# Performance work log

Hardware: AMD Instinct MI355X
Metric: run time of the kernel (lower is better)

## Reference

```python
import jax, jax.numpy as jnp
import numpy as np

B, C, H, W = 2, 256, 48, 48
NH = 8
HD = C // NH  # 32
T = H * W    # 2304


def setup_inputs() -> dict:
    keys = jax.random.split(jax.random.key(0), 16)
    s = lambda fan: 1.0 / np.sqrt(fan)
    x = jax.random.normal(keys[0], (B, C, H, W), jnp.float32)
    wq = jax.random.normal(keys[1], (C, C), jnp.float32) * s(C)
    bq = jax.random.normal(keys[2], (C,), jnp.float32) * 0.01
    wk = jax.random.normal(keys[3], (C, C), jnp.float32) * s(C)
    bk = jax.random.normal(keys[4], (C,), jnp.float32) * 0.01
    wv = jax.random.normal(keys[5], (C, C), jnp.float32) * s(C)
    bv = jax.random.normal(keys[6], (C,), jnp.float32) * 0.01
    wo = jax.random.normal(keys[7], (C, C), jnp.float32) * s(C)
    bo = jax.random.normal(keys[8], (C,), jnp.float32) * 0.01
    gamma1 = jnp.ones((C,), jnp.float32)
    beta1 = jnp.zeros((C,), jnp.float32)
    w1 = jax.random.normal(keys[9], (4 * C, C), jnp.float32) * s(C)
    bf1 = jax.random.normal(keys[10], (4 * C,), jnp.float32) * 0.01
    w2 = jax.random.normal(keys[11], (C, 4 * C), jnp.float32) * s(4 * C)
    bf2 = jax.random.normal(keys[12], (C,), jnp.float32) * 0.01
    gamma2 = jnp.ones((C,), jnp.float32)
    beta2 = jnp.zeros((C,), jnp.float32)
    return dict(x=x, wq=wq, bq=bq, wk=wk, bk=bk, wv=wv, bv=bv, wo=wo, bo=bo,
                gamma1=gamma1, beta1=beta1, w1=w1, bf1=bf1, w2=w2, bf2=bf2,
                gamma2=gamma2, beta2=beta2)


def group_norm1(x, gamma, beta, eps=1e-5):
    # GroupNorm(1, C): normalize over (C, H, W) per sample, per-channel affine.
    mu = jnp.mean(x, axis=(1, 2, 3), keepdims=True)
    var = jnp.mean((x - mu) ** 2, axis=(1, 2, 3), keepdims=True)
    xn = (x - mu) * jax.lax.rsqrt(var + eps)
    return xn * gamma[None, :, None, None] + beta[None, :, None, None]


def reference(x, wq, bq, wk, bk, wv, bv, wo, bo, gamma1, beta1,
              w1, bf1, w2, bf2, gamma2, beta2):
    b, c, h, w = x.shape
    t = h * w
    xt = x.reshape(b, c, t).transpose(0, 2, 1)  # [b, t, c]
    # 1x1 conv == per-token linear
    def heads(y):
        return y.reshape(b, t, NH, HD).transpose(0, 2, 1, 3)  # [b, nh, t, hd]
    q = heads(xt @ wq.T + bq)
    k = heads(xt @ wk.T + bk)
    v = heads(xt @ wv.T + bv)
    # flash SDPA runs in fp16 with fp32 accumulation
    q16 = q.astype(jnp.float16)
    k16 = k.astype(jnp.float16)
    v16 = v.astype(jnp.float16)
    scale = 1.0 / np.sqrt(HD)
    scores = jnp.einsum('bhqd,bhkd->bhqk', q16.astype(jnp.float32),
                        k16.astype(jnp.float32)) * scale
    attn = jax.nn.softmax(scores, axis=-1)
    out = jnp.einsum('bhqk,bhkd->bhqd', attn,
                     v16.astype(jnp.float32)).astype(jnp.float16)
    # remove component along normalized v (fp16, like torch code)
    vn = v16 / jnp.maximum(
        jnp.sqrt(jnp.sum(v16 * v16, axis=-1, keepdims=True)),
        jnp.float16(1e-12))
    out = out - jnp.sum(out * vn, axis=-1, keepdims=True) * vn
    out = out.astype(x.dtype)
    out = out.transpose(0, 2, 1, 3).reshape(b, t, c)  # [b, t, c]
    out = out @ wo.T + bo
    out = out.transpose(0, 2, 1).reshape(b, c, h, w)
    x1 = group_norm1(x + out, gamma1, beta1)
    # FFN: 1x1 conv -> relu -> 1x1 conv, per token
    x1t = x1.reshape(b, c, t).transpose(0, 2, 1)  # [b, t, c]
    hdn = jax.nn.relu(x1t @ w1.T + bf1)
    ffn = (hdn @ w2.T + bf2).transpose(0, 2, 1).reshape(b, c, h, w)
    x2 = group_norm1(x1 + ffn, gamma2, beta2)
    return x2
```

## Files before the change

### kernel.cpp

```cpp
#include <hip/hip_runtime.h>
#include <hip/hip_fp16.h>

typedef _Float16 f16x8 __attribute__((ext_vector_type(8)));
typedef __fp16 fp16x2 __attribute__((ext_vector_type(2)));
typedef float f32x4 __attribute__((ext_vector_type(4)));

namespace {

constexpr int B = 2, C = 256, T = 2304, F = 1024, NH = 8, HD = 32;
constexpr int BH = B * NH;
constexpr int NCHUNK = 4;
constexpr int CHUNK = T / NCHUNK;
constexpr float C2 = 0.17677669529663687f * 1.4426950408889634f;
constexpr float INV_N = 1.0f / (float)(C * T);

constexpr size_t N_WQKV = (size_t)3 * C * C;
constexpr size_t N_WO   = (size_t)C * C;
constexpr size_t N_W1   = (size_t)F * C;
constexpr size_t N_W2   = (size_t)C * F;
constexpr size_t N_WALL = N_WQKV + N_WO + N_W1 + N_W2;

constexpr size_t OFF_QKV  = 0;
constexpr size_t SZ_QKV   = (size_t)B * 3 * C * T * 2;
constexpr size_t OFF_AO   = OFF_QKV + SZ_QKV;
constexpr size_t SZ_AO    = (size_t)B * C * T * 2;
constexpr size_t OFF_X1   = OFF_AO + SZ_AO;
constexpr size_t SZ_X1    = (size_t)B * C * T * 4;
constexpr size_t OFF_PART = OFF_X1 + SZ_X1;
constexpr size_t SZ_OP    = (size_t)NCHUNK * BH * HD * T * 2;
constexpr size_t SZ_MP    = (size_t)NCHUNK * BH * T * 4;
constexpr size_t OFF_OP   = OFF_PART;
constexpr size_t OFF_MP   = OFF_OP + SZ_OP;
constexpr size_t OFF_LP   = OFF_MP + SZ_MP;
constexpr size_t SZ_H16   = (size_t)B * F * T * 2;
constexpr size_t SZ_PART  = SZ_OP + 2 * SZ_MP;
constexpr size_t SZ_UNION = SZ_PART > SZ_H16 ? SZ_PART : SZ_H16;
constexpr size_t OFF_H16  = OFF_PART;
constexpr size_t OFF_W16  = OFF_PART + SZ_UNION;
constexpr size_t OFF_BQKV = OFF_W16 + N_WALL * 2;
constexpr size_t OFF_STATS = OFF_BQKV + (size_t)3 * C * 4;

}

__global__ __launch_bounds__(256)
void convert_weights(const float* __restrict__ wq, const float* __restrict__ wk,
                     const float* __restrict__ wv, const float* __restrict__ wo,
                     const float* __restrict__ w1, const float* __restrict__ w2,
                     const float* __restrict__ bq, const float* __restrict__ bk,
                     const float* __restrict__ bv,
                     _Float16* __restrict__ w16, float* __restrict__ bqkv,
                     float* __restrict__ stats)
{
  const size_t tid = (size_t)blockIdx.x * 256 + threadIdx.x;
  if (tid < 8) stats[tid] = 0.f;
  if (tid < 3 * C)
    bqkv[tid] = tid < C ? bq[tid] : (tid < 2 * C ? bk[tid - C] : bv[tid - 2 * C]);
  for (size_t i4 = tid; i4 < N_WALL / 4; i4 += (size_t)gridDim.x * 256) {
    const size_t e = i4 * 4;
    const float* src;
    if      (e < 65536)  src = wq + e;
    else if (e < 131072) src = wk + (e - 65536);
    else if (e < 196608) src = wv + (e - 131072);
    else if (e < 262144) src = wo + (e - 196608);
    else if (e < 524288) src = w1 + (e - 262144);
    else                 src = w2 + (e - 524288);
    const float4 v = *(const float4*)src;
    union { _Float16 h[4]; uint2 u; } pk;
    pk.h[0] = (_Float16)v.x; pk.h[1] = (_Float16)v.y;
    pk.h[2] = (_Float16)v.z; pk.h[3] = (_Float16)v.w;
    *(uint2*)(w16 + e) = pk.u;
  }
}

template<bool RELU, bool RES, bool GNIN, bool GNRES, bool STATS,
         typename InT, typename OutT>
__global__ __launch_bounds__(256)
void gemm_mfma(const _Float16* __restrict__ W, const InT* __restrict__ X,
               const float* __restrict__ bias, const float* __restrict__ res,
               OutT* __restrict__ out, int CO, int K,
               const float* __restrict__ stats_in,
               const float* __restrict__ gamma, const float* __restrict__ beta,
               float* __restrict__ stats_out)
{
  const int b   = blockIdx.z;
  const int co0 = blockIdx.y * 64;
  const int t0  = blockIdx.x * 64;
  const int tid = threadIdx.x;
  const int wid = tid >> 6, lane = tid & 63;
  const int g = lane >> 4, lo = lane & 15;
  const int wm = wid & 1, wn = wid >> 1;

  __shared__ f16x8 xs[2][4][64];
  __shared__ float gs[256], bs[256];
  __shared__ float red[8];

  float mu = 0.f, rsig = 0.f;
  if (GNIN || GNRES) {
    const float s1 = stats_in[b * 2], s2 = stats_in[b * 2 + 1];
    mu = s1 * INV_N;
    rsig = rsqrtf(s2 * INV_N - mu * mu + 1e-5f);
  }
  if (GNIN) { gs[tid] = gamma[tid]; bs[tid] = beta[tid]; }

  const f32x4 z4 = {0.f, 0.f, 0.f, 0.f};
  f32x4 acc00 = z4, acc01 = z4, acc10 = z4, acc11 = z4;

  const int st = tid & 63;
  const int kp = tid >> 6;
  const InT* Xp = X + (size_t)b * K * T + t0 + st;
  const _Float16* Wp = W + (size_t)(co0 + wm * 32 + lo) * K + 8 * g;

  float xr[8];
#pragma unroll
  for (int j = 0; j < 8; ++j) xr[j] = (float)Xp[(size_t)(kp * 8 + j) * T];
  f16x8 afc0 = *(const f16x8*)(Wp);
  f16x8 afc1 = *(const f16x8*)(Wp + (size_t)16 * K);

  __syncthreads();

  int it = 0;
  for (int k0 = 0; k0 < K; k0 += 32, ++it) {
    const int buf = it & 1;
    union { fp16x2 h2[4]; f16x8 v8; } u;
#pragma unroll
    for (int j2 = 0; j2 < 4; ++j2) {
      float v0 = xr[2 * j2], v1 = xr[2 * j2 + 1];
      if (GNIN) {
        const int k = k0 + kp * 8 + 2 * j2;
        v0 = (v0 - mu) * rsig * gs[k] + bs[k];
        v1 = (v1 - mu) * rsig * gs[k + 1] + bs[k + 1];
      }
      u.h2[j2] = __builtin_amdgcn_cvt_pkrtz(v0, v1);
    }
    xs[buf][kp][st] = u.v8;

    const int k1 = (k0 + 32 < K) ? k0 + 32 : k0;
#pragma unroll
    for (int j = 0; j < 8; ++j) xr[j] = (float)Xp[(size_t)(k1 + kp * 8 + j) * T];
    const f16x8 afn0 = *(const f16x8*)(Wp + (size_t)k1);
    const f16x8 afn1 = *(const f16x8*)(Wp + (size_t)16 * K + k1);

    __syncthreads();

    const f16x8 bf0 = xs[buf][g][wn * 32 + lo];
    const f16x8 bf1 = xs[buf][g][wn * 32 + 16 + lo];
    acc00 = __builtin_amdgcn_mfma_f32_16x16x32_f16(afc0, bf0, acc00, 0, 0, 0);
    acc01 = __builtin_amdgcn_mfma_f32_16x16x32_f16(afc0, bf1, acc01, 0, 0, 0);
    acc10 = __builtin_amdgcn_mfma_f32_16x16x32_f16(afc1, bf0, acc10, 0, 0, 0);
    acc11 = __builtin_amdgcn_mfma_f32_16x16x32_f16(afc1, bf1, acc11, 0, 0, 0);

    afc0 = afn0;
    afc1 = afn1;
  }

  float s = 0.f, ss = 0.f;
  const size_t obase = ((size_t)b * CO + co0 + wm * 32) * T + t0 + wn * 32 + lo;
  const float* resb = res + obase;
  OutT* outb = out + obase;
  const f32x4 accs[2][2] = {{acc00, acc01}, {acc10, acc11}};
#pragma unroll
  for (int mi = 0; mi < 2; ++mi) {
#pragma unroll
    for (int r = 0; r < 4; ++r) {
      const int row = mi * 16 + 4 * g + r;
      const int co = co0 + wm * 32 + row;
      const float bi = bias[co];
      float gm = 0.f, bt = 0.f;
      if (GNRES) { gm = gamma[co]; bt = beta[co]; }
#pragma unroll
      for (int ni = 0; ni < 2; ++ni) {
        float v = accs[mi][ni][r] + bi;
        if (RES) {
          float rv = resb[(size_t)row * T + ni * 16];
          if (GNRES) rv = (rv - mu) * rsig * gm + bt;
          v += rv;
        }
        if (RELU) v = fmaxf(v, 0.f);
        outb[(size_t)row * T + ni * 16] = (OutT)v;
        if (STATS) { s += v; ss = fmaf(v, v, ss); }
      }
    }
  }

  if (STATS) {
#pragma unroll
    for (int off = 32; off > 0; off >>= 1) {
      s  += __shfl_down(s, off);
      ss += __shfl_down(ss, off);
    }
    if (lane == 0) { red[wid] = s; red[4 + wid] = ss; }
    __syncthreads();
    if (tid == 0) {
      atomicAdd(&stats_out[b * 2],     red[0] + red[1] + red[2] + red[3]);
      atomicAdd(&stats_out[b * 2 + 1], red[4] + red[5] + red[6] + red[7]);
    }
  }
}

__global__ __launch_bounds__(512)
void attn_mfma(const _Float16* __restrict__ qkv, _Float16* __restrict__ opart,
               float* __restrict__ mpart, float* __restrict__ lpart)
{
  const int tid  = threadIdx.x;
  const int wid  = tid >> 6;
  const int lane = tid & 63;
  const int g    = lane >> 4;
  const int lo   = lane & 15;
  const int chunk = blockIdx.y;
  const int bh   = blockIdx.z;
  const int b    = bh >> 3, h = bh & 7;
  const int tq   = blockIdx.x * 128 + wid * 16 + lo;
  const size_t qb = ((size_t)b * 3 * C + h * HD) * T;
  const size_t kb = qb + (size_t)C * T;
  const size_t vb = qb + (size_t)2 * C * T;

  __shared__ _Float16 kt[2][64][36];
  __shared__ _Float16 vt[2][32][72];
  __shared__ _Float16 pl[8][16][72];

  const int t   = tid & 63;
  const int dp  = tid >> 6;
  const int dv  = tid >> 4;
  const int seg = tid & 15;

  f16x8 qf;
#pragma unroll
  for (int j = 0; j < 8; ++j)
    qf[j] = (_Float16)((float)qkv[qb + (size_t)(8 * g + j) * T + tq] * C2);

  const f32x4 zero4 = {0.f, 0.f, 0.f, 0.f};
  f32x4 oa[2] = {zero4, zero4};
  float m = -1e30f, l = 0.f;

  constexpr int NIT = CHUNK / 64;

  ushort ka[4];
  uint2  va;
  {
    const int tk0 = chunk * CHUNK;
#pragma unroll
    for (int dd = 0; dd < 4; ++dd)
      ka[dd] = *(const ushort*)(qkv + kb + (size_t)(dp * 4 + dd) * T + tk0 + t);
    va = *(const uint2*)(qkv + vb + (size_t)dv * T + tk0 + seg * 4);
  }

  for (int it = 0; it < NIT; ++it) {
    const int buf = it & 1;

    *(uint*)&kt[buf][t][dp * 4]     = (uint)ka[0] | ((uint)ka[1] << 16);
    *(uint*)&kt[buf][t][dp * 4 + 2] = (uint)ka[2] | ((uint)ka[3] << 16);
    *(uint2*)&vt[buf][dv][seg * 4] = va;

    {
      const int tkn = chunk * CHUNK + (it + 1 < NIT ? it + 1 : it) * 64;
      ushort ka2[4];
      uint2  va2;
#pragma unroll
      for (int dd = 0; dd < 4; ++dd)
        ka2[dd] = *(const ushort*)(qkv + kb + (size_t)(dp * 4 + dd) * T + tkn + t);
      va2 = *(const uint2*)(qkv + vb + (size_t)dv * T + tkn + seg * 4);

      __syncthreads();

      f32x4 s4[4];
#pragma unroll
      for (int mt = 0; mt < 4; ++mt) {
        union { f16x8 v; uint2 u[2]; } kf;
        const _Float16* kr = &kt[buf][mt * 16 + lo][8 * g];
        kf.u[0] = *(const uint2*)(kr);
        kf.u[1] = *(const uint2*)(kr + 4);
        s4[mt] = __builtin_amdgcn_mfma_f32_16x16x32_f16(kf.v, qf, zero4, 0, 0, 0);
      }
      float rmax = -1e30f;
#pragma unroll
      for (int mt = 0; mt < 4; ++mt) {
        const float m01 = fmaxf(s4[mt][0], s4[mt][1]);
        const float m23 = fmaxf(s4[mt][2], s4[mt][3]);
        rmax = fmaxf(rmax, fmaxf(m01, m23));
      }
      rmax = fmaxf(rmax, __shfl_xor(rmax, 16));
      rmax = fmaxf(rmax, __shfl_xor(rmax, 32));
      if (!__all(rmax <= m)) {
        const float mn = fmaxf(m, rmax);
        const float fsc = __builtin_amdgcn_exp2f(m - mn);
        m = mn;
        l *= fsc;
#pragma unroll
        for (int dt = 0; dt < 2; ++dt)
#pragma unroll
          for (int r = 0; r < 4; ++r) oa[dt][r] *= fsc;
      }
      float p[4][4];
      float psum = 0.f;
#pragma unroll
      for (int mt = 0; mt < 4; ++mt)
#pragma unroll
        for (int r = 0; r < 4; ++r) {
          p[mt][r] = __builtin_amdgcn_exp2f(s4[mt][r] - m);
          psum += p[mt][r];
        }
      psum += __shfl_xor(psum, 16);
      psum += __shfl_xor(psum, 32);
      l += psum;

#pragma unroll
      for (int mt = 0; mt < 4; ++mt) {
        union { fp16x2 h2[2]; uint2 u2; } pw;
        pw.h2[0] = __builtin_amdgcn_cvt_pkrtz(p[mt][0], p[mt][1]);
        pw.h2[1] = __builtin_amdgcn_cvt_pkrtz(p[mt][2], p[mt][3]);
        *(uint2*)&pl[wid][lo][16 * mt + 4 * g] = pw.u2;
      }
#pragma unroll
      for (int c2 = 0; c2 < 2; ++c2) {
        const f16x8 pbv = *(const f16x8*)&pl[wid][lo][c2 * 32 + 8 * g];
#pragma unroll
        for (int dt = 0; dt < 2; ++dt) {
          const f16x8 vf = *(const f16x8*)&vt[buf][dt * 16 + lo][c2 * 32 + 8 * g];
          oa[dt] = __builtin_amdgcn_mfma_f32_16x16x32_f16(vf, pbv, oa[dt], 0, 0, 0);
        }
      }

#pragma unroll
      for (int dd = 0; dd < 4; ++dd) ka[dd] = ka2[dd];
      va = va2;
    }
  }

  const float invL = 1.f / l;
  const size_t ob = (size_t)(chunk * BH + bh) * HD * T;
#pragma unroll
  for (int dt = 0; dt < 2; ++dt)
#pragma unroll
    for (int r = 0; r < 4; ++r)
      opart[ob + (size_t)(dt * 16 + 4 * g + r) * T + tq] =
          (_Float16)(oa[dt][r] * invL);
  if (g == 0) {
    const size_t pb = (size_t)(chunk * BH + bh) * T + tq;
    mpart[pb] = m;
    lpart[pb] = l;
  }
}

__global__ __launch_bounds__(64)
void attn_combine(const _Float16* __restrict__ opart, const float* __restrict__ mpart,
                  const float* __restrict__ lpart, const _Float16* __restrict__ qkv,
                  _Float16* __restrict__ AOh)
{
  const int q  = blockIdx.x * 64 + threadIdx.x;
  const int bh = blockIdx.y;
  const int b  = bh >> 3, h = bh & 7;
  float mv[NCHUNK], lv[NCHUNK];
  float M = -1e30f;
#pragma unroll
  for (int c = 0; c < NCHUNK; ++c) {
    const size_t pb = (size_t)(c * BH + bh) * T + q;
    mv[c] = mpart[pb];
    lv[c] = lpart[pb];
    M = fmaxf(M, mv[c]);
  }
  float L = 0.f;
  float wc[NCHUNK];
#pragma unroll
  for (int c = 0; c < NCHUNK; ++c) {
    wc[c] = __builtin_amdgcn_exp2f(mv[c] - M) * lv[c];
    L += wc[c];
  }
  const float inv = 1.f / L;
#pragma unroll
  for (int c = 0; c < NCHUNK; ++c) wc[c] *= inv;

  float o[HD];
#pragma unroll
  for (int d = 0; d < HD; ++d) o[d] = 0.f;
#pragma unroll
  for (int c = 0; c < NCHUNK; ++c) {
    const size_t ob = (size_t)(c * BH + bh) * HD * T + q;
#pragma unroll
    for (int d = 0; d < HD; ++d)
      o[d] = fmaf(wc[c], (float)opart[ob + (size_t)d * T], o[d]);
  }

  const size_t vbase = ((size_t)b * 3 * C + 2 * C + h * HD) * T + q;
  float vv[HD], nrm2 = 0.f;
#pragma unroll
  for (int d = 0; d < HD; ++d) {
    vv[d] = (float)qkv[vbase + (size_t)d * T];
    nrm2 = fmaf(vv[d], vv[d], nrm2);
  }
  const float nrm = fmaxf(sqrtf(nrm2), 1e-12f);
  float dot = 0.f;
  float o16[HD], vn[HD];
#pragma unroll
  for (int d = 0; d < HD; ++d) {
    o16[d] = (float)(_Float16)(o[d]);
    vn[d]  = (float)(_Float16)(vv[d] / nrm);
    dot = fmaf(o16[d], vn[d], dot);
  }
  const size_t ab = ((size_t)b * C + h * HD) * T + q;
#pragma unroll
  for (int d = 0; d < HD; ++d)
    AOh[ab + (size_t)d * T] = (_Float16)(o16[d] - dot * vn[d]);
}

__global__ __launch_bounds__(256)
void gn_norm(const float* __restrict__ Y, const float* __restrict__ stats,
             const float* __restrict__ gamma, const float* __restrict__ beta,
             float* __restrict__ O)
{
  const int i = blockIdx.x * 256 + threadIdx.x;
  const int b = i / (C * T);
  const int c = (i / T) & (C - 1);
  const float mu  = stats[b * 2] * INV_N;
  const float var = stats[b * 2 + 1] * INV_N - mu * mu;
  const float r = rsqrtf(var + 1e-5f);
  O[i] = (Y[i] - mu) * r * gamma[c] + beta[c];
}

extern "C" void kernel_launch(void* const* d_in, const int* in_sizes, int n_in,
                              void* d_out, int out_size, void* d_ws, size_t ws_size,
                              hipStream_t stream)
{
  const float* x      = (const float*)d_in[0];
  const float* wq     = (const float*)d_in[1];
  const float* bq     = (const float*)d_in[2];
  const float* wk     = (const float*)d_in[3];
  const float* bk     = (const float*)d_in[4];
  const float* wv     = (const float*)d_in[5];
  const float* bv     = (const float*)d_in[6];
  const float* wo     = (const float*)d_in[7];
  const float* bo     = (const float*)d_in[8];
  const float* gamma1 = (const float*)d_in[9];
  const float* beta1  = (const float*)d_in[10];
  const float* w1     = (const float*)d_in[11];
  const float* bf1    = (const float*)d_in[12];
  const float* w2     = (const float*)d_in[13];
  const float* bf2    = (const float*)d_in[14];
  const float* gamma2 = (const float*)d_in[15];
  const float* beta2  = (const float*)d_in[16];

  char* ws = (char*)d_ws;
  _Float16* qkv16 = (_Float16*)(ws + OFF_QKV);
  _Float16* ao16  = (_Float16*)(ws + OFF_AO);
  float*    x1    = (float*)(ws + OFF_X1);
  _Float16* opart = (_Float16*)(ws + OFF_OP);
  float*    mpart = (float*)(ws + OFF_MP);
  float*    lpart = (float*)(ws + OFF_LP);
  _Float16* h16   = (_Float16*)(ws + OFF_H16);
  _Float16* w16   = (_Float16*)(ws + OFF_W16);
  float*    bqkv  = (float*)(ws + OFF_BQKV);
  float*    stats = (float*)(ws + OFF_STATS);
  float*    out   = (float*)d_out;

  const _Float16* wqkv16 = w16;
  const _Float16* wo16   = w16 + N_WQKV;
  const _Float16* w116   = w16 + N_WQKV + N_WO;
  const _Float16* w216   = w16 + N_WQKV + N_WO + N_W1;

  const dim3 blk256(256);

  convert_weights<<<768, blk256, 0, stream>>>(wq, wk, wv, wo, w1, w2, bq, bk, bv,
                                              w16, bqkv, stats);

  gemm_mfma<false, false, false, false, false, float, _Float16>
      <<<dim3(36, 12, 2), blk256, 0, stream>>>(
          wqkv16, x, bqkv, nullptr, qkv16, 3 * C, C, nullptr, nullptr, nullptr, nullptr);

  attn_mfma<<<dim3(T / 128, NCHUNK, BH), dim3(512), 0, stream>>>(qkv16, opart, mpart, lpart);
  attn_combine<<<dim3(T / 64, BH), dim3(64), 0, stream>>>(opart, mpart, lpart, qkv16, ao16);

  gemm_mfma<false, true, false, false, true, _Float16, float>
      <<<dim3(36, 4, 2), blk256, 0, stream>>>(
          wo16, ao16, bo, x, x1, C, C, nullptr, nullptr, nullptr, stats);

  gemm_mfma<true, false, true, false, false, float, _Float16>
      <<<dim3(36, 16, 2), blk256, 0, stream>>>(
          w116, x1, bf1, nullptr, h16, F, C, stats, gamma1, beta1, nullptr);

  gemm_mfma<false, true, false, true, true, _Float16, float>
      <<<dim3(36, 4, 2), blk256, 0, stream>>>(
          w216, h16, bf2, x1, out, C, F, stats, gamma1, beta1, stats + 4);

  gn_norm<<<dim3(4608), blk256, 0, stream>>>(out, stats + 4, gamma2, beta2, out);
}
```

Before: 125.3 us.

## Drop weight-conversion kernel, convert fp32 weights in GEMM; retile small GEMMs

Removes the separate convert_weights launch. Each GEMM now reads fp32 weights directly and packs them to fp16 in registers before the MFMA, and the QKV GEMM picks wq/wk/wv per block so no concatenated buffer is needed. Stats zeroing moves into attn_combine. The two CO=256 GEMMs switch to 32-token tiles for twice as many blocks, and attention split-K goes from 4 to 6 chunks. The cost is that every GEMM block reads twice the weight bytes and does redundant conversions.

```diff
diff --git a/kernel.cpp b/kernel.cpp
--- a/kernel.cpp
+++ b/kernel.cpp
@@ -9,16 +9,10 @@
 
 constexpr int B = 2, C = 256, T = 2304, F = 1024, NH = 8, HD = 32;
 constexpr int BH = B * NH;
-constexpr int NCHUNK = 4;
+constexpr int NCHUNK = 6;
 constexpr int CHUNK = T / NCHUNK;
 constexpr float C2 = 0.17677669529663687f * 1.4426950408889634f;
 constexpr float INV_N = 1.0f / (float)(C * T);
-
-constexpr size_t N_WQKV = (size_t)3 * C * C;
-constexpr size_t N_WO   = (size_t)C * C;
-constexpr size_t N_W1   = (size_t)F * C;
-constexpr size_t N_W2   = (size_t)C * F;
-constexpr size_t N_WALL = N_WQKV + N_WO + N_W1 + N_W2;
 
 constexpr size_t OFF_QKV  = 0;
 constexpr size_t SZ_QKV   = (size_t)B * 3 * C * T * 2;
@@ -36,61 +30,43 @@
 constexpr size_t SZ_PART  = SZ_OP + 2 * SZ_MP;
 constexpr size_t SZ_UNION = SZ_PART > SZ_H16 ? SZ_PART : SZ_H16;
 constexpr size_t OFF_H16  = OFF_PART;
-constexpr size_t OFF_W16  = OFF_PART + SZ_UNION;
-constexpr size_t OFF_BQKV = OFF_W16 + N_WALL * 2;
-constexpr size_t OFF_STATS = OFF_BQKV + (size_t)3 * C * 4;
-
-}
-
+constexpr size_t OFF_STATS = OFF_PART + SZ_UNION;
+
+__device__ inline f16x8 cvt8(const float4 a, const float4 b)
+{
+  union { fp16x2 h2[4]; f16x8 v; } u;
+  u.h2[0] = __builtin_amdgcn_cvt_pkrtz(a.x, a.y);
+  u.h2[1] = __builtin_amdgcn_cvt_pkrtz(a.z, a.w);
+  u.h2[2] = __builtin_amdgcn_cvt_pkrtz(b.x, b.y);
+  u.h2[3] = __builtin_amdgcn_cvt_pkrtz(b.z, b.w);
+  return u.v;
+}
+
+}
+
+template<int TT, bool QKV3, bool RELU, bool RES, bool GNIN, bool GNRES,
+         bool STATS, typename InT, typename OutT>
 __global__ __launch_bounds__(256)
-void convert_weights(const float* __restrict__ wq, const float* __restrict__ wk,
-                     const float* __restrict__ wv, const float* __restrict__ wo,
-                     const float* __restrict__ w1, const float* __restrict__ w2,
-                     const float* __restrict__ bq, const float* __restrict__ bk,
-                     const float* __restrict__ bv,
-                     _Float16* __restrict__ w16, float* __restrict__ bqkv,
-                     float* __restrict__ stats)
-{
-  const size_t tid = (size_t)blockIdx.x * 256 + threadIdx.x;
-  if (tid < 8) stats[tid] = 0.f;
-  if (tid < 3 * C)
-    bqkv[tid] = tid < C ? bq[tid] : (tid < 2 * C ? bk[tid - C] : bv[tid - 2 * C]);
-  for (size_t i4 = tid; i4 < N_WALL / 4; i4 += (size_t)gridDim.x * 256) {
-    const size_t e = i4 * 4;
-    const float* src;
-    if      (e < 65536)  src = wq + e;
-    else if (e < 131072) src = wk + (e - 65536);
-    else if (e < 196608) src = wv + (e - 131072);
-    else if (e < 262144) src = wo + (e - 196608);
-    else if (e < 524288) src = w1 + (e - 262144);
-    else                 src = w2 + (e - 524288);
-    const float4 v = *(const float4*)src;
-    union { _Float16 h[4]; uint2 u; } pk;
-    pk.h[0] = (_Float16)v.x; pk.h[1] = (_Float16)v.y;
-    pk.h[2] = (_Float16)v.z; pk.h[3] = (_Float16)v.w;
-    *(uint2*)(w16 + e) = pk.u;
-  }
-}
-
-template<bool RELU, bool RES, bool GNIN, bool GNRES, bool STATS,
-         typename InT, typename OutT>
-__global__ __launch_bounds__(256)
-void gemm_mfma(const _Float16* __restrict__ W, const InT* __restrict__ X,
-               const float* __restrict__ bias, const float* __restrict__ res,
+void gemm_mfma(const float* __restrict__ W0, const float* __restrict__ W1,
+               const float* __restrict__ W2, const InT* __restrict__ X,
+               const float* __restrict__ b0, const float* __restrict__ b1,
+               const float* __restrict__ b2, const float* __restrict__ res,
                OutT* __restrict__ out, int CO, int K,
                const float* __restrict__ stats_in,
                const float* __restrict__ gamma, const float* __restrict__ beta,
                float* __restrict__ stats_out)
 {
+  constexpr int TPS = TT / 8;
+  constexpr int NI  = TT / 32;
   const int b   = blockIdx.z;
   const int co0 = blockIdx.y * 64;
-  const int t0  = blockIdx.x * 64;
+  const int t0  = blockIdx.x * TT;
   const int tid = threadIdx.x;
   const int wid = tid >> 6, lane = tid & 63;
   const int g = lane >> 4, lo = lane & 15;
   const int wm = wid & 1, wn = wid >> 1;
 
-  __shared__ f16x8 xs[2][4][64];
+  __shared__ f16x8 xs[2][4][TT];
   __shared__ float gs[256], bs[256];
   __shared__ float red[8];
 
@@ -102,74 +78,105 @@
   }
   if (GNIN) { gs[tid] = gamma[tid]; bs[tid] = beta[tid]; }
 
+  const float* Wsel = W0;
+  const float* bsel = b0;
+  int cob = co0;
+  if (QKV3) {
+    if (co0 >= 512)      { Wsel = W2; bsel = b2; cob = co0 - 512; }
+    else if (co0 >= 256) { Wsel = W1; bsel = b1; cob = co0 - 256; }
+  }
+
   const f32x4 z4 = {0.f, 0.f, 0.f, 0.f};
-  f32x4 acc00 = z4, acc01 = z4, acc10 = z4, acc11 = z4;
-
-  const int st = tid & 63;
-  const int kp = tid >> 6;
+  f32x4 acc[2][2] = {{z4, z4}, {z4, z4}};
+
+  const int st = tid % TT;
+  const int kp = tid / TT;
   const InT* Xp = X + (size_t)b * K * T + t0 + st;
-  const _Float16* Wp = W + (size_t)(co0 + wm * 32 + lo) * K + 8 * g;
-
-  float xr[8];
-#pragma unroll
-  for (int j = 0; j < 8; ++j) xr[j] = (float)Xp[(size_t)(kp * 8 + j) * T];
-  f16x8 afc0 = *(const f16x8*)(Wp);
-  f16x8 afc1 = *(const f16x8*)(Wp + (size_t)16 * K);
+  const float* Wp = Wsel + (size_t)(cob + wm * 32 + lo) * K + 8 * g;
+
+  float xr[TPS];
+#pragma unroll
+  for (int j = 0; j < TPS; ++j) xr[j] = (float)Xp[(size_t)(kp * TPS + j) * T];
+  float4 wa[4];
+  wa[0] = *(const float4*)(Wp);
+  wa[1] = *(const float4*)(Wp + 4);
+  wa[2] = *(const float4*)(Wp + (size_t)16 * K);
+  wa[3] = *(const float4*)(Wp + (size_t)16 * K + 4);
 
   __syncthreads();
 
   int it = 0;
   for (int k0 = 0; k0 < K; k0 += 32, ++it) {
     const int buf = it & 1;
-    union { fp16x2 h2[4]; f16x8 v8; } u;
-#pragma unroll
-    for (int j2 = 0; j2 < 4; ++j2) {
-      float v0 = xr[2 * j2], v1 = xr[2 * j2 + 1];
-      if (GNIN) {
-        const int k = k0 + kp * 8 + 2 * j2;
-        v0 = (v0 - mu) * rsig * gs[k] + bs[k];
-        v1 = (v1 - mu) * rsig * gs[k + 1] + bs[k + 1];
-      }
-      u.h2[j2] = __builtin_amdgcn_cvt_pkrtz(v0, v1);
-    }
-    xs[buf][kp][st] = u.v8;
+    if constexpr (TT == 64) {
+      union { fp16x2 h2[4]; f16x8 v8; } u;
+#pragma unroll
+      for (int j2 = 0; j2 < 4; ++j2) {
+        float v0 = xr[2 * j2], v1 = xr[2 * j2 + 1];
+        if (GNIN) {
+          const int k = k0 + kp * 8 + 2 * j2;
+          v0 = (v0 - mu) * rsig * gs[k] + bs[k];
+          v1 = (v1 - mu) * rsig * gs[k + 1] + bs[k + 1];
+        }
+        u.h2[j2] = __builtin_amdgcn_cvt_pkrtz(v0, v1);
+      }
+      xs[buf][kp][st] = u.v8;
+    } else {
+      union { fp16x2 h2[2]; uint2 u2; } u;
+#pragma unroll
+      for (int j2 = 0; j2 < 2; ++j2) {
+        float v0 = xr[2 * j2], v1 = xr[2 * j2 + 1];
+        if (GNIN) {
+          const int k = k0 + kp * 4 + 2 * j2;
+          v0 = (v0 - mu) * rsig * gs[k] + bs[k];
+          v1 = (v1 - mu) * rsig * gs[k + 1] + bs[k + 1];
+        }
+        u.h2[j2] = __builtin_amdgcn_cvt_pkrtz(v0, v1);
+      }
+      *(uint2*)((_Float16*)&xs[buf][kp >> 1][st] + (kp & 1) * 4) = u.u2;
+    }
 
     const int k1 = (k0 + 32 < K) ? k0 + 32 : k0;
 #pragma unroll
-    for (int j = 0; j < 8; ++j) xr[j] = (float)Xp[(size_t)(k1 + kp * 8 + j) * T];
-    const f16x8 afn0 = *(const f16x8*)(Wp + (size_t)k1);
-    const f16x8 afn1 = *(const f16x8*)(Wp + (size_t)16 * K + k1);
+    for (int j = 0; j < TPS; ++j)
+      xr[j] = (float)Xp[(size_t)(k1 + kp * TPS + j) * T];
+    float4 wnx[4];
+    wnx[0] = *(const float4*)(Wp + k1);
+    wnx[1] = *(const float4*)(Wp + k1 + 4);
+    wnx[2] = *(const float4*)(Wp + (size_t)16 * K + k1);
+    wnx[3] = *(const float4*)(Wp + (size_t)16 * K + k1 + 4);
 
     __syncthreads();
 
-    const f16x8 bf0 = xs[buf][g][wn * 32 + lo];
-    const f16x8 bf1 = xs[buf][g][wn * 32 + 16 + lo];
-    acc00 = __builtin_amdgcn_mfma_f32_16x16x32_f16(afc0, bf0, acc00, 0, 0, 0);
-    acc01 = __builtin_amdgcn_mfma_f32_16x16x32_f16(afc0, bf1, acc01, 0, 0, 0);
-    acc10 = __builtin_amdgcn_mfma_f32_16x16x32_f16(afc1, bf0, acc10, 0, 0, 0);
-    acc11 = __builtin_amdgcn_mfma_f32_16x16x32_f16(afc1, bf1, acc11, 0, 0, 0);
-
-    afc0 = afn0;
-    afc1 = afn1;
+    const f16x8 afc0 = cvt8(wa[0], wa[1]);
+    const f16x8 afc1 = cvt8(wa[2], wa[3]);
+#pragma unroll
+    for (int ni = 0; ni < NI; ++ni) {
+      const f16x8 bf = xs[buf][g][wn * (TT / 2) + ni * 16 + lo];
+      acc[0][ni] = __builtin_amdgcn_mfma_f32_16x16x32_f16(afc0, bf, acc[0][ni], 0, 0, 0);
+      acc[1][ni] = __builtin_amdgcn_mfma_f32_16x16x32_f16(afc1, bf, acc[1][ni], 0, 0, 0);
+    }
+
+#pragma unroll
+    for (int q = 0; q < 4; ++q) wa[q] = wnx[q];
   }
 
   float s = 0.f, ss = 0.f;
-  const size_t obase = ((size_t)b * CO + co0 + wm * 32) * T + t0 + wn * 32 + lo;
+  const size_t obase = ((size_t)b * CO + co0 + wm * 32) * T + t0 + wn * (TT / 2) + lo;
   const float* resb = res + obase;
   OutT* outb = out + obase;
-  const f32x4 accs[2][2] = {{acc00, acc01}, {acc10, acc11}};
 #pragma unroll
   for (int mi = 0; mi < 2; ++mi) {
 #pragma unroll
     for (int r = 0; r < 4; ++r) {
       const int row = mi * 16 + 4 * g + r;
       const int co = co0 + wm * 32 + row;
-      const float bi = bias[co];
+      const float bi = bsel[cob + wm * 32 + row];
       float gm = 0.f, bt = 0.f;
       if (GNRES) { gm = gamma[co]; bt = beta[co]; }
 #pragma unroll
-      for (int ni = 0; ni < 2; ++ni) {
-        float v = accs[mi][ni][r] + bi;
+      for (int ni = 0; ni < NI; ++ni) {
+        float v = acc[mi][ni][r] + bi;
         if (RES) {
           float rv = resb[(size_t)row * T + ni * 16];
           if (GNRES) rv = (rv - mu) * rsig * gm + bt;
@@ -344,8 +351,10 @@
 __global__ __launch_bounds__(64)
 void attn_combine(const _Float16* __restrict__ opart, const float* __restrict__ mpart,
                   const float* __restrict__ lpart, const _Float16* __restrict__ qkv,
-                  _Float16* __restrict__ AOh)
-{
+                  _Float16* __restrict__ AOh, float* __restrict__ stats)
+{
+  if (blockIdx.x == 0 && blockIdx.y == 0 && threadIdx.x < 8)
+    stats[threadIdx.x] = 0.f;
   const int q  = blockIdx.x * 64 + threadIdx.x;
   const int bh = blockIdx.y;
   const int b  = bh >> 3, h = bh & 7;
@@ -446,39 +455,33 @@
   float*    mpart = (float*)(ws + OFF_MP);
   float*    lpart = (float*)(ws + OFF_LP);
   _Float16* h16   = (_Float16*)(ws + OFF_H16);
-  _Float16* w16   = (_Float16*)(ws + OFF_W16);
-  float*    bqkv  = (float*)(ws + OFF_BQKV);
   float*    stats = (float*)(ws + OFF_STATS);
   float*    out   = (float*)d_out;
 
-  const _Float16* wqkv16 = w16;
-  const _Float16* wo16   = w16 + N_WQKV;
-  const _Float16* w116   = w16 + N_WQKV + N_WO;
-  const _Float16* w216   = w16 + N_WQKV + N_WO + N_W1;
-
   const dim3 blk256(256);
 
-  convert_weights<<<768, blk256, 0, stream>>>(wq, wk, wv, wo, w1, w2, bq, bk, bv,
-                                              w16, bqkv, stats);
-
-  gemm_mfma<false, false, false, false, false, float, _Float16>
+  gemm_mfma<64, true, false, false, false, false, false, float, _Float16>
       <<<dim3(36, 12, 2), blk256, 0, stream>>>(
-          wqkv16, x, bqkv, nullptr, qkv16, 3 * C, C, nullptr, nullptr, nullptr, nullptr);
+          wq, wk, wv, x, bq, bk, bv, nullptr, qkv16, 3 * C, C,
+          nullptr, nullptr, nullptr, nullptr);
 
   attn_mfma<<<dim3(T / 128, NCHUNK, BH), dim3(512), 0, stream>>>(qkv16, opart, mpart, lpart);
-  attn_combine<<<dim3(T / 64, BH), dim3(64), 0, stream>>>(opart, mpart, lpart, qkv16, ao16);
-
-  gemm_mfma<false, true, false, false, true, _Float16, float>
-      <<<dim3(36, 4, 2), blk256, 0, stream>>>(
-          wo16, ao16, bo, x, x1, C, C, nullptr, nullptr, nullptr, stats);
-
-  gemm_mfma<true, false, true, false, false, float, _Float16>
+  attn_combine<<<dim3(T / 64, BH), dim3(64), 0, stream>>>(opart, mpart, lpart, qkv16, ao16, stats);
+
+  gemm_mfma<32, false, false, true, false, false, true, _Float16, float>
+      <<<dim3(72, 4, 2), blk256, 0, stream>>>(
+          wo, wo, wo, ao16, bo, bo, bo, x, x1, C, C,
+          nullptr, nullptr, nullptr, stats);
+
+  gemm_mfma<64, false, true, false, true, false, false, float, _Float16>
       <<<dim3(36, 16, 2), blk256, 0, stream>>>(
-          w116, x1, bf1, nullptr, h16, F, C, stats, gamma1, beta1, nullptr);
-
-  gemm_mfma<false, true, false, true, true, _Float16, float>
-      <<<dim3(36, 4, 2), blk256, 0, stream>>>(
-          w216, h16, bf2, x1, out, C, F, stats, gamma1, beta1, stats + 4);
+          w1, w1, w1, x1, bf1, bf1, bf1, nullptr, h16, F, C,
+          stats, gamma1, beta1, nullptr);
+
+  gemm_mfma<32, false, false, true, false, true, true, _Float16, float>
+      <<<dim3(72, 4, 2), blk256, 0, stream>>>(
+          w2, w2, w2, h16, bf2, bf2, bf2, x1, out, C, F,
+          stats, gamma1, beta1, stats + 4);
 
   gn_norm<<<dim3(4608), blk256, 0, stream>>>(out, stats + 4, gamma2, beta2, out);
 }
```

Measured after the change: 211.7 us. +68.9%, slower.
